# Performance work log

Hardware: AMD Instinct MI355X
Metric: run time of the kernel (lower is better)

Reference implementation:

```python
import jax, jax.numpy as jnp
import numpy as np

R = 8
TOP_K_A = 2
TOP_K_B = 2
SCALING = 16.0 / R  # lora_alpha / r


def setup_inputs() -> dict:
    key = jax.random.key(0)
    k1, k2, k3, k4, k5 = jax.random.split(key, 5)
    B, S, D_IN, D_OUT, EA, EB = 4, 2048, 4096, 4096, 8, 8
    x = jax.random.normal(k1, (B, S, D_IN), dtype=jnp.float32)
    router_logits_a = jax.random.normal(k2, (B * S, EA), dtype=jnp.float32)
    router_logits_b = jax.random.normal(k3, (B * S, EB), dtype=jnp.float32)
    # nn.Linear(in, r).weight -> [r, in]; stacked per expert: [E_a, r, in]
    Wa = jax.random.normal(k4, (EA, R, D_IN), dtype=jnp.float32) * (1.0 / np.sqrt(D_IN))
    # nn.Linear(r, out).weight -> [out, r]; stacked: [E_b, out, r]
    Wb = jax.random.normal(k5, (EB, D_OUT, R), dtype=jnp.float32) * (1.0 / np.sqrt(R))
    return {"x": x, "router_logits_a": router_logits_a,
            "router_logits_b": router_logits_b, "Wa": Wa, "Wb": Wb}


def reference(x, router_logits_a, router_logits_b, Wa, Wb):
    B, S, D_IN = x.shape
    flat_x = x.reshape(-1, D_IN)  # [T, D_in]

    # --- A experts: dense compute over all experts, then top-k gather ---
    topk_logits_a, topk_idx_a = jax.lax.top_k(router_logits_a, TOP_K_A)
    weights_a = jax.nn.softmax(topk_logits_a, axis=-1)  # [T, k_a]
    a_all = jnp.einsum('ti,eri->ter', flat_x, Wa)  # [T, E_a, r]
    sel_a = jnp.take_along_axis(a_all, topk_idx_a[:, :, None], axis=1)  # [T, k_a, r]
    mid = jnp.sum(sel_a * weights_a[:, :, None], axis=1)  # [T, r]

    # --- B experts: dense compute over all experts, then top-k gather ---
    b_all = jnp.einsum('tr,eor->teo', mid, Wb)  # [T, E_b, D_out]
    topk_logits_b, topk_idx_b = jax.lax.top_k(router_logits_b, TOP_K_B)
    weights_b = jax.nn.softmax(topk_logits_b, axis=-1)  # [T, k_b]
    sel_b = jnp.take_along_axis(b_all, topk_idx_b[:, :, None], axis=1)  # [T, k_b, D_out]
    out_flat = jnp.sum(sel_b * weights_b[:, :, None], axis=1) * SCALING  # [T, D_out]
    output = out_flat.reshape(B, S, -1)

    # --- load-balancing aux losses (torch.var is unbiased) ---
    probs_a = jnp.mean(jax.nn.softmax(router_logits_a, axis=-1), axis=0)
    probs_b = jnp.mean(jax.nn.softmax(router_logits_b, axis=-1), axis=0)
    aux_loss_a = Wa.shape[0] * jnp.var(probs_a, ddof=1)
    aux_loss_b = Wb.shape[0] * jnp.var(probs_b, ddof=1)
    return output, aux_loss_a, aux_loss_b
```

## Files before the change

kernel.cpp:

```cpp
#include <hip/hip_runtime.h>

#define T_TOK 8192
#define D_IN  4096
#define D_OUT 4096

typedef _Float16 h2 __attribute__((ext_vector_type(2)));
typedef _Float16 h4 __attribute__((ext_vector_type(4)));
typedef _Float16 h8 __attribute__((ext_vector_type(8)));
typedef float    f4v __attribute__((ext_vector_type(4)));

__device__ __forceinline__ h2 pkrtz(float a, float b) {
    auto r = __builtin_amdgcn_cvt_pkrtz(a, b);
    h2 o; __builtin_memcpy(&o, &r, 4); return o;
}
__device__ __forceinline__ h8 cvt8(float4 f0, float4 f1) {
    h2 p0 = pkrtz(f0.x, f0.y), p1 = pkrtz(f0.z, f0.w);
    h2 p2 = pkrtz(f1.x, f1.y), p3 = pkrtz(f1.z, f1.w);
    return (h8){p0.x, p0.y, p1.x, p1.y, p2.x, p2.y, p3.x, p3.y};
}
__device__ __forceinline__ h8 as_h8(uint4 u) { h8 b; __builtin_memcpy(&b, &u, 16); return b; }


__global__ __launch_bounds__(256)
void prep(const float* __restrict__ Wa, const float* __restrict__ Wb,
          const float* __restrict__ la, const float* __restrict__ lb,
          _Float16* __restrict__ WaB, _Float16* __restrict__ WbB,
          double* __restrict__ pax) {
    const int bid = blockIdx.x, tx = threadIdx.x;
    __shared__ double red[4][16];
    if (bid < 256) {
        int gid = bid * 256 + tx;
        int er = gid >> 10, k0 = (gid & 1023) * 4;
        float4 v = ((const float4*)Wa)[gid];
        h2 p0 = pkrtz(v.x, v.y), p1 = pkrtz(v.z, v.w);
        h4 o = { p0.x, p0.y, p1.x, p1.y };
        *(h4*)(WaB + ((k0 >> 3) * 64 + er) * 8 + (k0 & 7)) = o;
    } else if (bid < 384) {
        int gid = (bid - 256) * 256 + tx;
        int e = gid >> 12, o = gid & 4095;
        const float4* p = (const float4*)(Wb + ((size_t)e * 4096 + o) * 8);
        h8 v = cvt8(p[0], p[1]);
        *(h8*)(WbB + ((size_t)e * 4096 + o) * 8) = v;
    } else {
        const int ab = bid - 384;
        const int t = ab * 256 + tx;
        double loc[16];
        {
            float l[8];
#pragma unroll
            for (int i = 0; i < 8; ++i) l[i] = la[(size_t)t * 8 + i];
            float m = l[0];
#pragma unroll
            for (int i = 1; i < 8; ++i) m = fmaxf(m, l[i]);
            float s = 0.f, e[8];
#pragma unroll
            for (int i = 0; i < 8; ++i) { e[i] = __expf(l[i] - m); s += e[i]; }
#pragma unroll
            for (int i = 0; i < 8; ++i) loc[i] = (double)(e[i] / s);
        }
        {
            float l[8];
#pragma unroll
            for (int i = 0; i < 8; ++i) l[i] = lb[(size_t)t * 8 + i];
            float m = l[0];
#pragma unroll
            for (int i = 1; i < 8; ++i) m = fmaxf(m, l[i]);
            float s = 0.f, e[8];
#pragma unroll
            for (int i = 0; i < 8; ++i) { e[i] = __expf(l[i] - m); s += e[i]; }
#pragma unroll
            for (int i = 0; i < 8; ++i) loc[8 + i] = (double)(e[i] / s);
        }
        const int lane = tx & 63, wid = tx >> 6;
#pragma unroll
        for (int v = 0; v < 16; ++v) {
            double s = loc[v];
#pragma unroll
            for (int off = 32; off > 0; off >>= 1) s += __shfl_down(s, off, 64);
            if (lane == 0) red[wid][v] = s;
        }
        __syncthreads();
        if (tx < 16)
            pax[ab * 16 + tx] = red[0][tx] + red[1][tx] + red[2][tx] + red[3][tx];
    }
}

__global__ __launch_bounds__(256)
void fused(const float* __restrict__ x, const _Float16* __restrict__ WaB,
           const _Float16* __restrict__ WbB, const float* __restrict__ la,
           const float* __restrict__ lb, float* __restrict__ out,
           const double* __restrict__ pax) {
    __shared__ float    pL[16][66];
    __shared__ _Float16 MbL[1024];
    __shared__ float    sW0[16], sW1[16], sCb[16][8];
    __shared__ int      sE0[16], sE1[16];
    __shared__ double   sl[16];

    const int tx = threadIdx.x, l = tx & 63, w = tx >> 6;
    const int mr = l & 15, kf = l >> 4;
    const int m0 = blockIdx.x * 16;
    const int er1 = w * 16 + mr;

    f4v acc = (f4v){0.f, 0.f, 0.f, 0.f};
    const float* xr = x + (size_t)(m0 + mr) * D_IN + kf * 8;
    const uint4* wa4 = (const uint4*)WaB;

    float4 A0[8], A1[8]; uint4 B0[4], B1[4];

#define LD1(Ad, Bd, IT) do {                                                   \
    const float* ap_ = xr + (IT) * 128;                                        \
    _Pragma("unroll") for (int ks_ = 0; ks_ < 4; ++ks_) {                      \
        Ad[2 * ks_]     = *(const float4*)(ap_ + ks_ * 32);                    \
        Ad[2 * ks_ + 1] = *(const float4*)(ap_ + ks_ * 32 + 4); }              \
    _Pragma("unroll") for (int ks_ = 0; ks_ < 4; ++ks_)                        \
        Bd[ks_] = wa4[(size_t)(((IT) * 16 + ks_ * 4 + kf) * 64) + er1];        \
  } while (0)

#define CMP1(As, Bs) do {                                                      \
    _Pragma("unroll") for (int ks_ = 0; ks_ < 4; ++ks_) {                      \
        h8 a_ = cvt8(As[2 * ks_], As[2 * ks_ + 1]);                            \
        acc = __builtin_amdgcn_mfma_f32_16x16x32_f16(a_, as_h8(Bs[ks_]), acc,  \
                                                     0, 0, 0); }               \
  } while (0)

    LD1(A0, B0, 0);
#pragma unroll 1
    for (int it = 0; it < 30; it += 2) {
        LD1(A1, B1, it + 1); CMP1(A0, B0);
        LD1(A0, B0, it + 2); CMP1(A1, B1);
    }
    LD1(A1, B1, 31); CMP1(A0, B0); CMP1(A1, B1);
#undef LD1
#undef CMP1

#pragma unroll
    for (int r = 0; r < 4; ++r) pL[kf * 4 + r][er1] = acc[r];
    __syncthreads();

    if (tx < 16) {
        const int t = tx;
        float lg[8];
#pragma unroll
        for (int i = 0; i < 8; ++i) lg[i] = la[(size_t)(m0 + t) * 8 + i];
        int e0 = 0; float b0 = lg[0];
#pragma unroll
        for (int i = 1; i < 8; ++i) if (lg[i] > b0) { b0 = lg[i]; e0 = i; }
        int e1 = -1; float b1 = -1e30f;
#pragma unroll
        for (int i = 0; i < 8; ++i) if (i != e0 && lg[i] > b1) { b1 = lg[i]; e1 = i; }
        float w1 = __expf(b1 - b0), s = 1.f + w1;
        sW0[t] = 1.f / s; sW1[t] = w1 / s; sE0[t] = e0; sE1[t] = e1;

#pragma unroll
        for (int i = 0; i < 8; ++i) lg[i] = lb[(size_t)(m0 + t) * 8 + i];
        int f0 = 0; float c0 = lg[0];
#pragma unroll
        for (int i = 1; i < 8; ++i) if (lg[i] > c0) { c0 = lg[i]; f0 = i; }
        int f1 = -1; float c1 = -1e30f;
#pragma unroll
        for (int i = 0; i < 8; ++i) if (i != f0 && lg[i] > c1) { c1 = lg[i]; f1 = i; }
        float wb1 = __expf(c1 - c0), sb = 1.f + wb1;
        float wb0s = 2.f / sb, wb1s = 2.f * wb1 / sb;
#pragma unroll
        for (int e = 0; e < 8; ++e)
            sCb[t][e] = (e == f0) ? wb0s : (e == f1) ? wb1s : 0.f;
    }
    __syncthreads();

    {
        const int t = tx >> 4, g = tx & 15;
        const float w0 = sW0[t], w1 = sW1[t];
        const int e0 = sE0[t], e1 = sE1[t];
        const float cb = sCb[t][g >> 1];
        h4 o;
#pragma unroll
        for (int j = 0; j < 4; ++j) {
            int r = (g * 4 + j) & 7;
            float mid = w0 * pL[t][e0 * 8 + r] + w1 * pL[t][e1 * 8 + r];
            o[j] = (_Float16)(cb * mid);
        }
        *(h4*)(MbL + ((g >> 1) * 16 + t) * 8 + (g & 1) * 4) = o;
    }
    __syncthreads();

    h8 a30, a31;
    a30 = *(const h8*)(MbL + ((0 * 4 + kf) * 16 + mr) * 8);
    a31 = *(const h8*)(MbL + ((1 * 4 + kf) * 16 + mr) * 8);
    const uint4* wb4 = (const uint4*)WbB;
    const size_t bofs0 = (size_t)((0 * 4 + kf) * 4096);
    const size_t bofs1 = (size_t)((1 * 4 + kf) * 4096);
    float* outp = out + (size_t)(m0 + kf * 4) * D_OUT;

    uint4 C0[4], C1[4];
#define LDB3(Cd, CH) do { int n0_ = (CH) * 128 + w * 32 + mr;                  \
    Cd[0] = wb4[bofs0 + n0_];      Cd[1] = wb4[bofs0 + n0_ + 16];              \
    Cd[2] = wb4[bofs1 + n0_];      Cd[3] = wb4[bofs1 + n0_ + 16];              \
  } while (0)

#define CMP3(Cs, CH) do {                                                      \
    f4v o0 = (f4v){0.f,0.f,0.f,0.f}, o1 = (f4v){0.f,0.f,0.f,0.f};              \
    o0 = __builtin_amdgcn_mfma_f32_16x16x32_f16(a30, as_h8(Cs[0]), o0, 0,0,0); \
    o0 = __builtin_amdgcn_mfma_f32_16x16x32_f16(a31, as_h8(Cs[2]), o0, 0,0,0); \
    o1 = __builtin_amdgcn_mfma_f32_16x16x32_f16(a30, as_h8(Cs[1]), o1, 0,0,0); \
    o1 = __builtin_amdgcn_mfma_f32_16x16x32_f16(a31, as_h8(Cs[3]), o1, 0,0,0); \
    int n0_ = (CH) * 128 + w * 32 + mr;                                        \
    _Pragma("unroll") for (int r_ = 0; r_ < 4; ++r_) {                         \
        outp[(size_t)r_ * D_OUT + n0_]      = o0[r_];                          \
        outp[(size_t)r_ * D_OUT + n0_ + 16] = o1[r_]; }                        \
  } while (0)

    LDB3(C0, 0);
#pragma unroll 1
    for (int c = 0; c < 30; c += 2) {
        LDB3(C1, c + 1); CMP3(C0, c);
        LDB3(C0, c + 2); CMP3(C1, c + 1);
    }
    LDB3(C1, 31); CMP3(C0, 30); CMP3(C1, 31);
#undef LDB3
#undef CMP3

    if (blockIdx.x == 0) {
        if (tx < 16) {
            double s = 0.0;
#pragma unroll
            for (int b = 0; b < 32; ++b) s += pax[b * 16 + tx];
            sl[tx] = s;
        }
        __syncthreads();
        if (tx == 0) {
            double pa[8], pb[8], ma = 0.0, mb = 0.0;
            for (int e = 0; e < 8; ++e) { pa[e] = sl[e] / 8192.0;     ma += pa[e] / 8.0; }
            for (int e = 0; e < 8; ++e) { pb[e] = sl[8 + e] / 8192.0; mb += pb[e] / 8.0; }
            double va = 0.0, vb = 0.0;
            for (int e = 0; e < 8; ++e) { double d = pa[e] - ma; va += d * d; }
            for (int e = 0; e < 8; ++e) { double d = pb[e] - mb; vb += d * d; }
            out[(size_t)T_TOK * D_OUT + 0] = (float)(8.0 * va / 7.0);
            out[(size_t)T_TOK * D_OUT + 1] = (float)(8.0 * vb / 7.0);
        }
    }
}

extern "C" void kernel_launch(void* const* d_in, const int* in_sizes, int n_in,
                              void* d_out, int out_size, void* d_ws, size_t ws_size,
                              hipStream_t stream) {
    const float* x  = (const float*)d_in[0];
    const float* la = (const float*)d_in[1];
    const float* lb = (const float*)d_in[2];
    const float* Wa = (const float*)d_in[3];
    const float* Wb = (const float*)d_in[4];
    float* out = (float*)d_out;

    char* ws = (char*)d_ws;
    _Float16* WaB = (_Float16*)ws;
    _Float16* WbB = (_Float16*)(ws + 524288);
    double*   pax = (double*)(ws + 1048576);

    prep<<<416, 256, 0, stream>>>(Wa, Wb, la, lb, WaB, WbB, pax);
    fused<<<512, 256, 0, stream>>>(x, WaB, WbB, la, lb, out, pax);
}
```

Before: 286.1 us.

## Stage x and expert weights through LDS via async global_load_lds double buffering

Replaces the register-prefetch pipelines in both GEMM phases with direct global-to-LDS loads (global_load_lds, 16 bytes per lane) into double-buffered shared memory. The x tile uses an XOR swizzle to avoid bank conflicts, and each stage is followed by __syncthreads. The aim is to cut register pressure and VGPR-level latency while keeping loads coalesced. In exchange it adds a large LDS footprint, about 48KB in a union, which may lower occupancy, and a block barrier on every iteration.

```diff
diff --git a/kernel.cpp b/kernel.cpp
--- a/kernel.cpp
+++ b/kernel.cpp
@@ -18,7 +18,12 @@
     h2 p2 = pkrtz(f1.x, f1.y), p3 = pkrtz(f1.z, f1.w);
     return (h8){p0.x, p0.y, p1.x, p1.y, p2.x, p2.y, p3.x, p3.y};
 }
-__device__ __forceinline__ h8 as_h8(uint4 u) { h8 b; __builtin_memcpy(&b, &u, 16); return b; }
+
+__device__ __forceinline__ void gl_lds16(const void* g, void* l) {
+    __builtin_amdgcn_global_load_lds(
+        (const __attribute__((address_space(1))) unsigned int*)g,
+        (__attribute__((address_space(3))) unsigned int*)l, 16, 0, 0);
+}
 
 
 __global__ __launch_bounds__(256)
@@ -90,6 +95,10 @@
            const _Float16* __restrict__ WbB, const float* __restrict__ la,
            const float* __restrict__ lb, float* __restrict__ out,
            const double* __restrict__ pax) {
+    __shared__ union {
+        struct { float xb[2][2048]; _Float16 wab[2][8192]; } p1;
+        struct { _Float16 wbb[2][8192]; } p3;
+    } U;
     __shared__ float    pL[16][66];
     __shared__ _Float16 MbL[1024];
     __shared__ float    sW0[16], sW1[16], sCb[16][8];
@@ -102,35 +111,47 @@
     const int er1 = w * 16 + mr;
 
     f4v acc = (f4v){0.f, 0.f, 0.f, 0.f};
-    const float* xr = x + (size_t)(m0 + mr) * D_IN + kf * 8;
-    const uint4* wa4 = (const uint4*)WaB;
-
-    float4 A0[8], A1[8]; uint4 B0[4], B1[4];
-
-#define LD1(Ad, Bd, IT) do {                                                   \
-    const float* ap_ = xr + (IT) * 128;                                        \
+
+#define STAGE1(IT, BUF) do {                                                   \
+    _Pragma("unroll") for (int i_ = 0; i_ < 2; ++i_) {                         \
+        int j_ = w * 2 + i_;                                                   \
+        int row_ = j_ * 2 + (l >> 5);                                          \
+        int cb_ = ((l & 31) * 16) ^ ((row_ & 7) << 4);                         \
+        const char* src_ = (const char*)x                                      \
+            + (((size_t)(m0 + row_) * D_IN + (size_t)(IT) * 128) << 2) + cb_;  \
+        gl_lds16(src_, (char*)U.p1.xb[BUF] + j_ * 1024);                       \
+    }                                                                          \
+    _Pragma("unroll") for (int i_ = 0; i_ < 4; ++i_) {                         \
+        int j_ = w * 4 + i_;                                                   \
+        const char* src_ = (const char*)WaB + (size_t)(IT) * 16384             \
+            + j_ * 1024 + l * 16;                                              \
+        gl_lds16(src_, (char*)U.p1.wab[BUF] + j_ * 1024);                      \
+    }                                                                          \
+  } while (0)
+
+#define CMP1(BUF) do {                                                         \
+    const char* xb_ = (const char*)U.p1.xb[BUF] + mr * 512;                    \
+    const int sw_ = (mr & 7) << 4;                                             \
     _Pragma("unroll") for (int ks_ = 0; ks_ < 4; ++ks_) {                      \
-        Ad[2 * ks_]     = *(const float4*)(ap_ + ks_ * 32);                    \
-        Ad[2 * ks_ + 1] = *(const float4*)(ap_ + ks_ * 32 + 4); }              \
-    _Pragma("unroll") for (int ks_ = 0; ks_ < 4; ++ks_)                        \
-        Bd[ks_] = wa4[(size_t)(((IT) * 16 + ks_ * 4 + kf) * 64) + er1];        \
-  } while (0)
-
-#define CMP1(As, Bs) do {                                                      \
-    _Pragma("unroll") for (int ks_ = 0; ks_ < 4; ++ks_) {                      \
-        h8 a_ = cvt8(As[2 * ks_], As[2 * ks_ + 1]);                            \
-        acc = __builtin_amdgcn_mfma_f32_16x16x32_f16(a_, as_h8(Bs[ks_]), acc,  \
-                                                     0, 0, 0); }               \
-  } while (0)
-
-    LD1(A0, B0, 0);
+        int c0_ = ks_ * 128 + kf * 32;                                         \
+        float4 f0_ = *(const float4*)(xb_ + ((c0_) ^ sw_));                    \
+        float4 f1_ = *(const float4*)(xb_ + ((c0_ + 16) ^ sw_));               \
+        h8 a_ = cvt8(f0_, f1_);                                                \
+        h8 b_ = *(const h8*)((const char*)U.p1.wab[BUF]                        \
+                             + ((ks_ * 4 + kf) * 64 + er1) * 16);              \
+        acc = __builtin_amdgcn_mfma_f32_16x16x32_f16(a_, b_, acc, 0, 0, 0);    \
+    }                                                                          \
+  } while (0)
+
+    STAGE1(0, 0);
+    __syncthreads();
 #pragma unroll 1
-    for (int it = 0; it < 30; it += 2) {
-        LD1(A1, B1, it + 1); CMP1(A0, B0);
-        LD1(A0, B0, it + 2); CMP1(A1, B1);
-    }
-    LD1(A1, B1, 31); CMP1(A0, B0); CMP1(A1, B1);
-#undef LD1
+    for (int it = 0; it < 32; ++it) {
+        if (it < 31) STAGE1(it + 1, (it & 1) ^ 1);
+        CMP1(it & 1);
+        __syncthreads();
+    }
+#undef STAGE1
 #undef CMP1
 
 #pragma unroll
@@ -168,55 +189,60 @@
     __syncthreads();
 
     {
-        const int t = tx >> 4, g = tx & 15;
+        const int t = tx >> 4, gg = tx & 15;
         const float w0 = sW0[t], w1 = sW1[t];
         const int e0 = sE0[t], e1 = sE1[t];
-        const float cb = sCb[t][g >> 1];
+        const float cb = sCb[t][gg >> 1];
         h4 o;
 #pragma unroll
         for (int j = 0; j < 4; ++j) {
-            int r = (g * 4 + j) & 7;
+            int r = (gg * 4 + j) & 7;
             float mid = w0 * pL[t][e0 * 8 + r] + w1 * pL[t][e1 * 8 + r];
             o[j] = (_Float16)(cb * mid);
         }
-        *(h4*)(MbL + ((g >> 1) * 16 + t) * 8 + (g & 1) * 4) = o;
-    }
-    __syncthreads();
-
-    h8 a30, a31;
-    a30 = *(const h8*)(MbL + ((0 * 4 + kf) * 16 + mr) * 8);
-    a31 = *(const h8*)(MbL + ((1 * 4 + kf) * 16 + mr) * 8);
-    const uint4* wb4 = (const uint4*)WbB;
-    const size_t bofs0 = (size_t)((0 * 4 + kf) * 4096);
-    const size_t bofs1 = (size_t)((1 * 4 + kf) * 4096);
+        *(h4*)(MbL + ((gg >> 1) * 16 + t) * 8 + (gg & 1) * 4) = o;
+    }
+    __syncthreads();
+
+    h8 a30 = *(const h8*)(MbL + ((0 * 4 + kf) * 16 + mr) * 8);
+    h8 a31 = *(const h8*)(MbL + ((1 * 4 + kf) * 16 + mr) * 8);
     float* outp = out + (size_t)(m0 + kf * 4) * D_OUT;
 
-    uint4 C0[4], C1[4];
-#define LDB3(Cd, CH) do { int n0_ = (CH) * 128 + w * 32 + mr;                  \
-    Cd[0] = wb4[bofs0 + n0_];      Cd[1] = wb4[bofs0 + n0_ + 16];              \
-    Cd[2] = wb4[bofs1 + n0_];      Cd[3] = wb4[bofs1 + n0_ + 16];              \
-  } while (0)
-
-#define CMP3(Cs, CH) do {                                                      \
+#define STAGE3(CH, BUF) do {                                                   \
+    _Pragma("unroll") for (int i_ = 0; i_ < 4; ++i_) {                         \
+        int j_ = w * 4 + i_;                                                   \
+        const char* src_ = (const char*)WbB + (size_t)(j_ >> 1) * 65536        \
+            + (size_t)(CH) * 2048 + (j_ & 1) * 1024 + l * 16;                  \
+        gl_lds16(src_, (char*)U.p3.wbb[BUF] + j_ * 1024);                      \
+    }                                                                          \
+  } while (0)
+
+#define CMP3(BUF, CH) do {                                                     \
     f4v o0 = (f4v){0.f,0.f,0.f,0.f}, o1 = (f4v){0.f,0.f,0.f,0.f};              \
-    o0 = __builtin_amdgcn_mfma_f32_16x16x32_f16(a30, as_h8(Cs[0]), o0, 0,0,0); \
-    o0 = __builtin_amdgcn_mfma_f32_16x16x32_f16(a31, as_h8(Cs[2]), o0, 0,0,0); \
-    o1 = __builtin_amdgcn_mfma_f32_16x16x32_f16(a30, as_h8(Cs[1]), o1, 0,0,0); \
-    o1 = __builtin_amdgcn_mfma_f32_16x16x32_f16(a31, as_h8(Cs[3]), o1, 0,0,0); \
+    _Pragma("unroll") for (int ks_ = 0; ks_ < 2; ++ks_) {                      \
+        const char* bb_ = (const char*)U.p3.wbb[BUF]                           \
+            + ((ks_ * 4 + kf) * 128 + w * 32 + mr) * 16;                       \
+        h8 b0_ = *(const h8*)(bb_);                                            \
+        h8 b1_ = *(const h8*)(bb_ + 256);                                      \
+        h8 af_ = ks_ ? a31 : a30;                                              \
+        o0 = __builtin_amdgcn_mfma_f32_16x16x32_f16(af_, b0_, o0, 0, 0, 0);    \
+        o1 = __builtin_amdgcn_mfma_f32_16x16x32_f16(af_, b1_, o1, 0, 0, 0);    \
+    }                                                                          \
     int n0_ = (CH) * 128 + w * 32 + mr;                                        \
     _Pragma("unroll") for (int r_ = 0; r_ < 4; ++r_) {                         \
         outp[(size_t)r_ * D_OUT + n0_]      = o0[r_];                          \
         outp[(size_t)r_ * D_OUT + n0_ + 16] = o1[r_]; }                        \
   } while (0)
 
-    LDB3(C0, 0);
+    STAGE3(0, 0);
+    __syncthreads();
 #pragma unroll 1
-    for (int c = 0; c < 30; c += 2) {
-        LDB3(C1, c + 1); CMP3(C0, c);
-        LDB3(C0, c + 2); CMP3(C1, c + 1);
-    }
-    LDB3(C1, 31); CMP3(C0, 30); CMP3(C1, 31);
-#undef LDB3
+    for (int c = 0; c < 32; ++c) {
+        if (c < 31) STAGE3(c + 1, (c & 1) ^ 1);
+        CMP3(c & 1, c);
+        __syncthreads();
+    }
+#undef STAGE3
 #undef CMP3
 
     if (blockIdx.x == 0) {
```

Result: faster. 269.3 us (-5.9%).
